# Kernel tuning notes

Measured on AMD Instinct MI355X. Metric: run time of the kernel, lower is better.

The kernel has to match this reference:

```python
import jax, jax.numpy as jnp
import numpy as np

B, S, T = 1024, 1024, 32  # batch, seq_len, num_tags


def setup_inputs() -> dict:
    key = jax.random.key(0)
    k1, k2, k3, k4 = jax.random.split(key, 4)
    logits = jax.random.normal(k1, (B, S, T), dtype=jnp.float32)
    transitions = jax.random.normal(k2, (T, T), dtype=jnp.float32)
    tags = jax.random.randint(k3, (B, S), 0, T)
    lengths = jax.random.randint(k4, (B,), 1, S + 1)
    return {"logits": logits, "transitions": transitions, "tags": tags, "lengths": lengths}


def _forward_alg(logits, transitions):
    # viterbi_0 = logits[:, 0, :]; then for t>=1:
    # v_next[b, j] = logsumexp_i(v[b, i] + trans[i, j]) + logits[b, t, j]
    v0 = logits[:, 0, :]  # (B, T)
    emits = jnp.swapaxes(logits[:, 1:, :], 0, 1)  # (S-1, B, T)

    def step(v, emit_t):
        v_next = jax.nn.logsumexp(v[:, :, None] + transitions[None, :, :], axis=1) + emit_t
        return v_next, None

    v_final, _ = jax.lax.scan(step, v0, emits)
    return jax.nn.logsumexp(v_final, axis=1)  # (B,)


def _score_sentence(logits, transitions, tags, lengths):
    # emission scores of gold tags, masked to t < length (note: original ignores
    # lengths in the forward algorithm but uses them here, faithfully reproduced)
    emit = jnp.take_along_axis(logits, tags[:, :, None], axis=2)[..., 0]  # (B, S)
    pos = jnp.arange(S)
    emit_mask = (pos[None, :] < lengths[:, None]).astype(logits.dtype)
    score = jnp.sum(emit * emit_mask, axis=1)
    # transition scores trans[tags[t-1], tags[t]] for 1 <= t < length
    trans_sc = transitions[tags[:, :-1], tags[:, 1:]]  # (B, S-1)
    trans_mask = (pos[None, 1:] < lengths[:, None]).astype(logits.dtype)
    score = score + jnp.sum(trans_sc * trans_mask, axis=1)
    return score  # (B,)


def reference(logits, transitions, tags, lengths):
    log_z = _forward_alg(logits, transitions)
    gold = _score_sentence(logits, transitions, tags, lengths)
    return jnp.mean(log_z - gold)
```

## Files before the change

### kernel.cpp

```cpp
#include <hip/hip_runtime.h>

#define NB 1024
#define NS 1024
#define NT 32
#define L2E 1.44269504088896340736f
#define LN2 0.69314718055994530942f

typedef short        bfrag  __attribute__((ext_vector_type(8)));
typedef float        cfrag  __attribute__((ext_vector_type(16)));
typedef __bf16       bf16x2 __attribute__((ext_vector_type(2)));
typedef float        f32x8  __attribute__((ext_vector_type(8)));
typedef float        f32x2  __attribute__((ext_vector_type(2)));
typedef unsigned int u32;
typedef unsigned int u32x4  __attribute__((ext_vector_type(4)));

__device__ __forceinline__ float fexp2(float x){ return __builtin_amdgcn_exp2f(x); }
__device__ __forceinline__ float flog2(float x){ return __builtin_amdgcn_logf(x); }
__device__ __forceinline__ float frcp (float x){ return __builtin_amdgcn_rcpf(x); }

__device__ __forceinline__ u32 pkbf(float a, float b){
    f32x2 t; t.x = a; t.y = b;
    return __builtin_bit_cast(u32, __builtin_convertvector(t, bf16x2));
}
__device__ __forceinline__ bfrag mk_afrag(f32x8 v){
    u32x4 r;
    r[0] = pkbf(v[0], v[1]); r[1] = pkbf(v[2], v[3]);
    r[2] = pkbf(v[4], v[5]); r[3] = pkbf(v[6], v[7]);
    return __builtin_bit_cast(bfrag, r);
}

__global__ __launch_bounds__(64, 4) void crf_chunk(
    const float* __restrict__ logits, const float* __restrict__ trans,
    const int* __restrict__ tags, const int* __restrict__ lens,
    u32* __restrict__ wmat, float* __restrict__ woff, float* __restrict__ wgold)
{
    const int tid = threadIdx.x;
    const int m = tid & 31, h = tid >> 5;
    const int bc = blockIdx.x;
    const int b = bc >> 3, c = bc & 7;

    const float* base = logits + (size_t)b * NS * NT;
    const int*   tgp  = tags + b * NS;
    const int    len  = lens[b];

    f32x8 Et0, Et1;
    #pragma unroll
    for (int j = 0; j < 8; j++){
        Et0[j] = fexp2(L2E * trans[(     8*h + j)*NT + m]);
        Et1[j] = fexp2(L2E * trans[(16 + 8*h + j)*NT + m]);
    }

    u32x4 B0v, B1v;
    #pragma unroll
    for (int d = 0; d < 4; d++){
        int k0 = 8*h + 2*d;      u32 v = 0;
        if (k0     == m) v |= 0x3F80u;
        if (k0 + 1 == m) v |= 0x3F800000u;
        B0v[d] = v;
        int k1 = 16 + 8*h + 2*d; v = 0;
        if (k1     == m) v |= 0x3F80u;
        if (k1 + 1 == m) v |= 0x3F800000u;
        B1v[d] = v;
    }

    cfrag zacc;
    #pragma unroll
    for (int q = 0; q < 16; q++) zacc[q] = 0.0f;

    float off = 0.0f;
    float gold = 0.0f;
    if (c == 0){
        float e0 = base[m];
        int  tag0 = tgp[0];
        gold += (h == 0 && m == tag0) ? e0 : 0.0f;
    }

    const int tbeg = c*128 + 1;
    const int tend = (c == 7) ? (NS - 1) : (c*128 + 128);
    const int L    = tend - tbeg + 1;

    float eA[8], eB[8]; int gA[8], gB[8];
    auto loadblk = [&](float (&e)[8], int (&g)[8], int k){
        #pragma unroll
        for (int i = 0; i < 8; i++){
            int t = tbeg + k*8 + i;
            t = t > (NS-1) ? (NS-1) : t;
            e[i] = base[t*NT + m];
            g[i] = tgp[t];
        }
    };

    auto step = [&](float e, int tagc, int t, bool renorm){
        float d = fexp2(e * L2E);
        bfrag A0 = mk_afrag(Et0 * d);
        bfrag A1 = mk_afrag(Et1 * d);
        cfrag acc = __builtin_amdgcn_mfma_f32_32x32x16_bf16(
                        A0, __builtin_bit_cast(bfrag, B0v), zacc, 0, 0, 0);
        acc = __builtin_amdgcn_mfma_f32_32x32x16_bf16(
                        A1, __builtin_bit_cast(bfrag, B1v), acc, 0, 0, 0);

        gold += (h == 0 && m == tagc && t < len) ? e : 0.0f;

        u32 P[8];
        if (renorm){
            float mx = acc[0];
            #pragma unroll
            for (int q = 1; q < 16; q++) mx = fmaxf(mx, acc[q]);
            mx = fmaxf(mx, __shfl_xor(mx, 32, 64));
            off += flog2(mx);
            float s = frcp(mx);
            #pragma unroll
            for (int i = 0; i < 8; i++) P[i] = pkbf(acc[2*i]*s, acc[2*i+1]*s);
        } else {
            #pragma unroll
            for (int i = 0; i < 8; i++) P[i] = pkbf(acc[2*i], acc[2*i+1]);
        }

        u32 X0 = __shfl_xor(h ? P[0] : P[2], 32, 64);
        u32 X1 = __shfl_xor(h ? P[1] : P[3], 32, 64);
        u32 X2 = __shfl_xor(h ? P[4] : P[6], 32, 64);
        u32 X3 = __shfl_xor(h ? P[5] : P[7], 32, 64);
        B0v[0] = h ? X0 : P[0];  B0v[1] = h ? X1 : P[1];
        B0v[2] = h ? P[2] : X0;  B0v[3] = h ? P[3] : X1;
        B1v[0] = h ? X2 : P[4];  B1v[1] = h ? X3 : P[5];
        B1v[2] = h ? P[6] : X2;  B1v[3] = h ? P[7] : X3;
    };

    loadblk(eA, gA, 0);
    const int nblk = 16;
    for (int k = 0; k < nblk; k += 2){
        loadblk(eB, gB, k + 1);
        {
            #pragma unroll
            for (int i = 0; i < 8; i++)
                step(eA[i], gA[i], tbeg + k*8 + i, (i & 3) == 3);
        }
        if (k + 2 < nblk) loadblk(eA, gA, k + 2);
        {
            const int nst = (L - (k+1)*8) >= 8 ? 8 : (L - (k+1)*8);
            #pragma unroll
            for (int i = 0; i < 8; i++)
                if (i < nst) step(eB[i], gB[i], tbeg + (k+1)*8 + i, (i & 3) == 3);
        }
    }

    const size_t mb = (size_t)bc * 512;
    #pragma unroll
    for (int d = 0; d < 4; d++){
        wmat[mb + d*64 + tid]     = B0v[d];
        wmat[mb + (4+d)*64 + tid] = B1v[d];
    }
    if (h == 0) woff[bc*32 + m] = off;

    #pragma unroll
    for (int d = 1; d <= 16; d <<= 1) gold += __shfl_xor(gold, d, 64);
    if (tid == 0) wgold[bc] = gold;
}

__global__ __launch_bounds__(64) void crf_combine(
    const float* __restrict__ logits, const float* __restrict__ trans,
    const int* __restrict__ tags, const int* __restrict__ lens,
    const u32* __restrict__ wmat, const float* __restrict__ woff,
    const float* __restrict__ wgold, float* __restrict__ out)
{
    __shared__ __align__(16) float ldsT[NT*NT];
    __shared__ __align__(16) int   ldsTag[NS];
    __shared__ __align__(16) float ldsU[NT];

    const int tid = threadIdx.x;
    const int m   = tid & 31;
    const int b   = blockIdx.x;
    const int len = lens[b];

    #pragma unroll
    for (int i = 0; i < 16; i++) ldsT[tid + i*64] = trans[tid + i*64];
    const int4* tg4 = (const int4*)(tags + b*NS);
    #pragma unroll
    for (int i = 0; i < 4; i++) ((int4*)ldsTag)[tid + i*64] = tg4[tid + i*64];
    __syncthreads();

    float g = 0.0f;
    #pragma unroll
    for (int it = 0; it < 16; it++){
        int t = 1 + tid + it*64;
        if (t < NS && t < len)
            g += ldsT[ldsTag[t-1]*NT + ldsTag[t]];
    }
    if (tid < 8) g += wgold[b*8 + tid];

    float v = fexp2(L2E * logits[(size_t)b*NS*NT + m]);
    float voff = 0.0f;

    const int n  = m;
    const int f  = n >> 4;
    const int hh = (n >> 3) & 1;
    const int di = f*4 + ((n >> 1) & 3);

    for (int cc = 0; cc < 8; cc++){
        const int bcn = b*8 + cc;
        float offm = woff[bcn*32 + m];
        float w = flog2(v) + offm;
        float mw = w;
        #pragma unroll
        for (int d = 1; d <= 16; d <<= 1) mw = fmaxf(mw, __shfl_xor(mw, d, 64));
        float u = fexp2(w - mw);
        if (tid < 32) ldsU[m] = u;
        __syncthreads();

        const uint4*  mp = (const uint4*)(wmat + (size_t)bcn*512 + di*64 + hh*32);
        float acc = 0.0f;
        #pragma unroll
        for (int qq = 0; qq < 8; qq++){
            uint4  md = mp[qq];
            float4 uu = ((const float4*)ldsU)[qq];
            float e0 = __builtin_bit_cast(float, (n&1) ? (md.x & 0xFFFF0000u) : (md.x << 16));
            float e1 = __builtin_bit_cast(float, (n&1) ? (md.y & 0xFFFF0000u) : (md.y << 16));
            float e2 = __builtin_bit_cast(float, (n&1) ? (md.z & 0xFFFF0000u) : (md.z << 16));
            float e3 = __builtin_bit_cast(float, (n&1) ? (md.w & 0xFFFF0000u) : (md.w << 16));
            acc = fmaf(e0, uu.x, acc);
            acc = fmaf(e1, uu.y, acc);
            acc = fmaf(e2, uu.z, acc);
            acc = fmaf(e3, uu.w, acc);
        }
        v = acc;
        voff += mw;
        __syncthreads();
    }

    float s = v;
    #pragma unroll
    for (int d = 1; d <= 16; d <<= 1) s += __shfl_xor(s, d, 64);
    #pragma unroll
    for (int d = 1; d <= 32; d <<= 1) g += __shfl_xor(g, d, 64);
    if (tid == 0){
        float logz = LN2 * (voff + flog2(s));
        atomicAdd(out, (logz - g) * (1.0f / (float)NB));
    }
}

extern "C" void kernel_launch(void* const* d_in, const int* in_sizes, int n_in,
                              void* d_out, int out_size, void* d_ws, size_t ws_size,
                              hipStream_t stream) {
    const float* logits = (const float*)d_in[0];
    const float* trans  = (const float*)d_in[1];
    const int*   tags   = (const int*)d_in[2];
    const int*   lens   = (const int*)d_in[3];

    u32*   wmat  = (u32*)d_ws;
    float* woff  = (float*)(wmat + 8192*512);
    float* wgold = woff + 8192*32;

    hipMemsetAsync(d_out, 0, sizeof(float), stream);
    crf_chunk  <<<8192, 64, 0, stream>>>(logits, trans, tags, lens, wmat, woff, wgold);
    crf_combine<<<1024, 64, 0, stream>>>(logits, trans, tags, lens, wmat, woff, wgold,
                                         (float*)d_out);
}
```

Baseline: 290.9 us.

## Apply emissions after MFMA via LDS, use permlane32 swap, raise occupancy

The emission factor is no longer folded into the A fragments on every step. The A fragments are now constant exp(trans) values, and each output column is scaled by exp(emit) after the MFMA. Those exp(emit) values are precomputed by both half-waves and staged in a double-buffered LDS array, replacing the per-step exp and bf16 repacking of A. The cross-half exchange uses permlane32_swap when the builtin is available, and launch bounds rise from 4 to 6 waves. This shortens the serial dependency chain per step at the cost of LDS reads and extra multiplies, and the result changes because scaling now happens in fp32 after the product rather than in bf16 before it.

```diff
diff --git a/kernel.cpp b/kernel.cpp
--- a/kernel.cpp
+++ b/kernel.cpp
@@ -12,6 +12,7 @@
 typedef float        f32x8  __attribute__((ext_vector_type(8)));
 typedef float        f32x2  __attribute__((ext_vector_type(2)));
 typedef unsigned int u32;
+typedef unsigned int u32x2v __attribute__((ext_vector_type(2)));
 typedef unsigned int u32x4  __attribute__((ext_vector_type(4)));
 
 __device__ __forceinline__ float fexp2(float x){ return __builtin_amdgcn_exp2f(x); }
@@ -29,11 +30,31 @@
     return __builtin_bit_cast(bfrag, r);
 }
 
-__global__ __launch_bounds__(64, 4) void crf_chunk(
+#if __has_builtin(__builtin_amdgcn_permlane32_swap)
+#define HAVE_PLSWAP 1
+#else
+#define HAVE_PLSWAP 0
+#endif
+
+__device__ __forceinline__ void half_swap(u32 &x, u32 &y, int h){
+#if HAVE_PLSWAP
+    u32x2v r = __builtin_amdgcn_permlane32_swap(x, y, false, false);
+    x = r[0]; y = r[1];
+#else
+    u32 X  = __shfl_xor(h ? x : y, 32, 64);
+    u32 nx = h ? X : x;
+    u32 ny = h ? y : X;
+    x = nx; y = ny;
+#endif
+}
+
+__global__ __launch_bounds__(64, 6) void crf_chunk(
     const float* __restrict__ logits, const float* __restrict__ trans,
     const int* __restrict__ tags, const int* __restrict__ lens,
     u32* __restrict__ wmat, float* __restrict__ woff, float* __restrict__ wgold)
 {
+    __shared__ __align__(16) float dsc[512];
+
     const int tid = threadIdx.x;
     const int m = tid & 31, h = tid >> 5;
     const int bc = blockIdx.x;
@@ -49,6 +70,8 @@
         Et0[j] = fexp2(L2E * trans[(     8*h + j)*NT + m]);
         Et1[j] = fexp2(L2E * trans[(16 + 8*h + j)*NT + m]);
     }
+    const bfrag A0f = mk_afrag(Et0);
+    const bfrag A1f = mk_afrag(Et1);
 
     u32x4 B0v, B1v;
     #pragma unroll
@@ -76,72 +99,82 @@
     }
 
     const int tbeg = c*128 + 1;
-    const int tend = (c == 7) ? (NS - 1) : (c*128 + 128);
-    const int L    = tend - tbeg + 1;
-
-    float eA[8], eB[8]; int gA[8], gB[8];
-    auto loadblk = [&](float (&e)[8], int (&g)[8], int k){
-        #pragma unroll
-        for (int i = 0; i < 8; i++){
-            int t = tbeg + k*8 + i;
-            t = t > (NS-1) ? (NS-1) : t;
+    const int L    = (c == 7) ? 127 : 128;
+
+    float eA[4], eB[4]; int gA[4], gB[4];
+
+    auto issue = [&](float (&e)[4], int (&g)[4], int k){
+        const int t0 = tbeg + k*8 + 4*h;
+        #pragma unroll
+        for (int i = 0; i < 4; i++){
+            int t = t0 + i; t = t > (NS-1) ? (NS-1) : t;
             e[i] = base[t*NT + m];
             g[i] = tgp[t];
         }
     };
-
-    auto step = [&](float e, int tagc, int t, bool renorm){
-        float d = fexp2(e * L2E);
-        bfrag A0 = mk_afrag(Et0 * d);
-        bfrag A1 = mk_afrag(Et1 * d);
-        cfrag acc = __builtin_amdgcn_mfma_f32_32x32x16_bf16(
-                        A0, __builtin_bit_cast(bfrag, B0v), zacc, 0, 0, 0);
-        acc = __builtin_amdgcn_mfma_f32_32x32x16_bf16(
-                        A1, __builtin_bit_cast(bfrag, B1v), acc, 0, 0, 0);
-
-        gold += (h == 0 && m == tagc && t < len) ? e : 0.0f;
-
-        u32 P[8];
-        if (renorm){
-            float mx = acc[0];
-            #pragma unroll
-            for (int q = 1; q < 16; q++) mx = fmaxf(mx, acc[q]);
-            mx = fmaxf(mx, __shfl_xor(mx, 32, 64));
-            off += flog2(mx);
-            float s = frcp(mx);
-            #pragma unroll
-            for (int i = 0; i < 8; i++) P[i] = pkbf(acc[2*i]*s, acc[2*i+1]*s);
-        } else {
-            #pragma unroll
-            for (int i = 0; i < 8; i++) P[i] = pkbf(acc[2*i], acc[2*i+1]);
+    auto commit = [&](float (&e)[4], int k){
+        float* sp = dsc + (k & 1)*256 + (4*h)*32 + m;
+        #pragma unroll
+        for (int i = 0; i < 4; i++) sp[i*32] = fexp2(L2E * e[i]);
+    };
+
+    auto proc = [&](float (&e)[4], int (&g)[4], int k){
+        const float* db = dsc + (k & 1)*256 + 4*h;
+        const int rem = L - k*8;
+        const int nst = rem >= 8 ? 8 : rem;
+        #pragma unroll
+        for (int i = 0; i < 8; i++){
+            if (i < nst){
+                const int t = tbeg + k*8 + i;
+                cfrag acc = __builtin_amdgcn_mfma_f32_32x32x16_bf16(
+                                A0f, __builtin_bit_cast(bfrag, B0v), zacc, 0, 0, 0);
+                acc = __builtin_amdgcn_mfma_f32_32x32x16_bf16(
+                                A1f, __builtin_bit_cast(bfrag, B1v), acc, 0, 0, 0);
+
+                float4 d0 = *(const float4*)(db + i*32 +  0);
+                float4 d1 = *(const float4*)(db + i*32 +  8);
+                float4 d2 = *(const float4*)(db + i*32 + 16);
+                float4 d3 = *(const float4*)(db + i*32 + 24);
+                acc[0]*=d0.x;  acc[1]*=d0.y;  acc[2]*=d0.z;  acc[3]*=d0.w;
+                acc[4]*=d1.x;  acc[5]*=d1.y;  acc[6]*=d1.z;  acc[7]*=d1.w;
+                acc[8]*=d2.x;  acc[9]*=d2.y;  acc[10]*=d2.z; acc[11]*=d2.w;
+                acc[12]*=d3.x; acc[13]*=d3.y; acc[14]*=d3.z; acc[15]*=d3.w;
+
+                const int li = i & 3;
+                if (h == (i >> 2) && m == g[li] && t < len) gold += e[li];
+
+                if ((i & 3) == 3){
+                    float mx = acc[0];
+                    #pragma unroll
+                    for (int q = 1; q < 16; q++) mx = fmaxf(mx, acc[q]);
+                    mx = fmaxf(mx, __shfl_xor(mx, 32, 64));
+                    off += flog2(mx);
+                    float s = frcp(mx);
+                    #pragma unroll
+                    for (int q = 0; q < 16; q++) acc[q] *= s;
+                }
+
+                u32 P0 = pkbf(acc[0], acc[1]),  P1 = pkbf(acc[2], acc[3]);
+                u32 P2 = pkbf(acc[4], acc[5]),  P3 = pkbf(acc[6], acc[7]);
+                u32 P4 = pkbf(acc[8], acc[9]),  P5 = pkbf(acc[10], acc[11]);
+                u32 P6 = pkbf(acc[12], acc[13]),P7 = pkbf(acc[14], acc[15]);
+                half_swap(P0, P2, h); half_swap(P1, P3, h);
+                half_swap(P4, P6, h); half_swap(P5, P7, h);
+                B0v[0]=P0; B0v[1]=P1; B0v[2]=P2; B0v[3]=P3;
+                B1v[0]=P4; B1v[1]=P5; B1v[2]=P6; B1v[3]=P7;
+            }
         }
-
-        u32 X0 = __shfl_xor(h ? P[0] : P[2], 32, 64);
-        u32 X1 = __shfl_xor(h ? P[1] : P[3], 32, 64);
-        u32 X2 = __shfl_xor(h ? P[4] : P[6], 32, 64);
-        u32 X3 = __shfl_xor(h ? P[5] : P[7], 32, 64);
-        B0v[0] = h ? X0 : P[0];  B0v[1] = h ? X1 : P[1];
-        B0v[2] = h ? P[2] : X0;  B0v[3] = h ? P[3] : X1;
-        B1v[0] = h ? X2 : P[4];  B1v[1] = h ? X3 : P[5];
-        B1v[2] = h ? P[6] : X2;  B1v[3] = h ? P[7] : X3;
     };
 
-    loadblk(eA, gA, 0);
-    const int nblk = 16;
-    for (int k = 0; k < nblk; k += 2){
-        loadblk(eB, gB, k + 1);
-        {
-            #pragma unroll
-            for (int i = 0; i < 8; i++)
-                step(eA[i], gA[i], tbeg + k*8 + i, (i & 3) == 3);
-        }
-        if (k + 2 < nblk) loadblk(eA, gA, k + 2);
-        {
-            const int nst = (L - (k+1)*8) >= 8 ? 8 : (L - (k+1)*8);
-            #pragma unroll
-            for (int i = 0; i < 8; i++)
-                if (i < nst) step(eB[i], gB[i], tbeg + (k+1)*8 + i, (i & 3) == 3);
-        }
+    issue(eA, gA, 0);
+    commit(eA, 0);
+    for (int k = 0; k < 16; k += 2){
+        issue(eB, gB, k + 1);
+        proc(eA, gA, k);
+        commit(eB, k + 1);
+        if (k + 2 < 16) issue(eA, gA, k + 2);
+        proc(eB, gB, k + 1);
+        if (k + 2 < 16) commit(eA, k + 2);
     }
 
     const size_t mb = (size_t)bc * 512;
```

After: 272.5 us. -6.3%, faster.
